# Kernel tuning notes

Measured on AMD Instinct MI355X. Metric: run time of the kernel, lower is better.

The kernel has to match this reference:

```python
import jax, jax.numpy as jnp
import numpy as np

N, F, K, O = 8192, 512, 2, 64
FMIN = jnp.finfo(jnp.float32).min


def setup_inputs() -> dict:
    key = jax.random.key(0)
    k1, k2, k3, k4, k5 = jax.random.split(key, 5)
    H = jax.random.normal(k1, (N, F), dtype=jnp.float32)
    # sparse-ish binary adjacency with self-loops (float mask, as in TF code)
    A = (jax.random.uniform(k2, (N, N)) < 0.0125).astype(jnp.float32)
    A = jnp.maximum(A, jnp.eye(N, dtype=jnp.float32))
    idx = jnp.arange(N, dtype=jnp.int32)
    W = jax.random.normal(k3, (K, F, O), dtype=jnp.float32) * 0.1
    b = jnp.zeros((K, O), dtype=jnp.float32)
    a1 = jax.random.normal(k4, (K, O), dtype=jnp.float32) * 0.1
    a2 = jax.random.normal(k5, (K, O), dtype=jnp.float32) * 0.1
    return {"H": H, "A": A, "idx": idx, "W": W, "b": b, "a1": a1, "a2": a2}


def reference(H, A, idx, W, b, a1, a2):
    # batch_A = tf.gather(A, idx, axis=1)
    batch_A = A[:, idx]                                  # [N, N]
    HW = jnp.einsum('nf,kfo->kno', H, W)                 # [K, N, O]
    attn1 = jnp.einsum('kno,ko->kn', HW, a1)             # [K, N]
    attn2 = jnp.einsum('kno,ko->kn', HW, a2)             # [K, N]
    # transpose(meshgrid sum): scores[k, i, j] = attn1[k, i] + attn2[k, j]
    scores = attn1[:, :, None] + attn2[:, None, :]       # [K, N, N]
    scores = scores + FMIN * (1.0 - batch_A)[None]
    scores = jnp.where(scores >= 0, scores, 0.2 * scores)  # LeakyReLU(0.2)
    attn = jax.nn.softmax(scores, axis=-1)               # [K, N, N]
    # res = transpose(HW^T @ attn) => res[k, i] = sum_j attn[k, j, i] * HW[k, j]
    res = jnp.einsum('kji,kjo->kio', attn, HW)           # [K, N, O]
    out = jax.nn.relu(res + b[:, None, :])               # [K, N, O]
    # concat heads along feature axis
    return jnp.transpose(out, (1, 0, 2)).reshape(N, K * O)
```

## Files before the change

### kernel.cpp

```cpp
#include <hip/hip_runtime.h>

#define NN 8192
#define FD 512
typedef unsigned long long u64;

__device__ __forceinline__ unsigned f2bf(float x) {
  unsigned u = __float_as_uint(x);
  u += 0x7FFFu + ((u >> 16) & 1u);
  return u >> 16;
}

__device__ __forceinline__ u64 xpose64(u64 x, int lane) {
  const u64 M[6] = {0x00000000FFFFFFFFULL, 0x0000FFFF0000FFFFULL,
                    0x00FF00FF00FF00FFULL, 0x0F0F0F0F0F0F0F0FULL,
                    0x3333333333333333ULL, 0x5555555555555555ULL};
  int d = 32;
#pragma unroll
  for (int s = 0; s < 6; ++s, d >>= 1) {
    u64 y = __shfl_xor(x, d);
    const u64 ML = M[s], MH = ~ML;
    if ((lane & d) == 0) x = (x & ML) | ((y & ML) << d);
    else                 x = (x & MH) | ((y & MH) >> d);
  }
  return x;
}

__global__ __launch_bounds__(256) void kA(
    const float* __restrict__ H, const float* __restrict__ W,
    const float* __restrict__ a1, const float* __restrict__ a2,
    const float* __restrict__ A, const int* __restrict__ idx,
    unsigned* __restrict__ hw2, float* __restrict__ c1,
    float* __restrict__ c2p, u64* __restrict__ rmask_t) {
  __shared__ u64 sm[4][128];
  __shared__ int sbad;
  const int wv = threadIdx.x >> 6, lane = threadIdx.x & 63;
  if (blockIdx.x < 512) {
    const int nbase = __builtin_amdgcn_readfirstlane(blockIdx.x * 16 + wv * 4);
    const float* __restrict__ W0 = W;
    const float* __restrict__ W1 = W + FD * 64;
    float acc0[4] = {0.f, 0.f, 0.f, 0.f};
    float acc1[4] = {0.f, 0.f, 0.f, 0.f};
    float4 hc[4], hn[4];
#pragma unroll
    for (int r = 0; r < 4; ++r)
      hc[r] = *(const float4*)(H + (size_t)(nbase + r) * FD);
    for (int f = 0; f < FD; f += 4) {
      if (f + 4 < FD) {
#pragma unroll
        for (int r = 0; r < 4; ++r)
          hn[r] = *(const float4*)(H + (size_t)(nbase + r) * FD + f + 4);
      }
      const float w00 = W0[(f+0)*64 + lane], w01 = W0[(f+1)*64 + lane];
      const float w02 = W0[(f+2)*64 + lane], w03 = W0[(f+3)*64 + lane];
      const float w10 = W1[(f+0)*64 + lane], w11 = W1[(f+1)*64 + lane];
      const float w12 = W1[(f+2)*64 + lane], w13 = W1[(f+3)*64 + lane];
#pragma unroll
      for (int r = 0; r < 4; ++r) {
        acc0[r] = fmaf(hc[r].x, w00, acc0[r]);
        acc0[r] = fmaf(hc[r].y, w01, acc0[r]);
        acc0[r] = fmaf(hc[r].z, w02, acc0[r]);
        acc0[r] = fmaf(hc[r].w, w03, acc0[r]);
        acc1[r] = fmaf(hc[r].x, w10, acc1[r]);
        acc1[r] = fmaf(hc[r].y, w11, acc1[r]);
        acc1[r] = fmaf(hc[r].z, w12, acc1[r]);
        acc1[r] = fmaf(hc[r].w, w13, acc1[r]);
      }
#pragma unroll
      for (int r = 0; r < 4; ++r) hc[r] = hn[r];
    }
    const float a10 = a1[lane],      a20 = a2[lane];
    const float a11 = a1[64 + lane], a21 = a2[64 + lane];
#pragma unroll
    for (int r = 0; r < 4; ++r) {
      const int n = nbase + r;
      hw2[(size_t)n * 64 + lane] = f2bf(acc0[r]) | (f2bf(acc1[r]) << 16);
      float s10 = acc0[r] * a10;
      float s20 = acc0[r] * a20;
      float s11 = acc1[r] * a11;
      float s21 = acc1[r] * a21;
#pragma unroll
      for (int off = 32; off; off >>= 1) {
        s10 += __shfl_down(s10, off);
        s20 += __shfl_down(s20, off);
        s11 += __shfl_down(s11, off);
        s21 += __shfl_down(s21, off);
      }
      if (lane == 0) {
        c1[n]          = s10;
        c1[NN + n]     = s11;
        c2p[n * 2]     = s20;
        c2p[n * 2 + 1] = s21;
      }
    }
    return;
  }
  const int bs = blockIdx.x - 512;
  const int j = bs * 4 + wv;
  if (threadIdx.x == 0) sbad = 0;
  __syncthreads();
  {
    bool bad = false;
    const int4* __restrict__ idx4 = (const int4*)idx;
#pragma unroll
    for (int p = 0; p < 8; ++p) {
      const int t = threadIdx.x + p * 256;
      const int4 v = idx4[t];
      const int b0 = t * 4;
      bad |= (v.x != b0) | (v.y != b0 + 1) | (v.z != b0 + 2) | (v.w != b0 + 3);
    }
    if (__ballot(bad) != 0ULL && lane == 0) sbad = 1;
  }
  __syncthreads();
  const bool fast = (sbad == 0);
  const float* __restrict__ Arow = A + (size_t)j * NN;

  float4 cur[4], nxt[4];
  {
    const int cb = lane * 4;
    if (fast) {
#pragma unroll
      for (int p = 0; p < 4; ++p) cur[p] = *(const float4*)(Arow + cb + p * 256);
    } else {
#pragma unroll
      for (int p = 0; p < 4; ++p) {
        const int c0 = cb + p * 256;
        cur[p].x = Arow[idx[c0 + 0]]; cur[p].y = Arow[idx[c0 + 1]];
        cur[p].z = Arow[idx[c0 + 2]]; cur[p].w = Arow[idx[c0 + 3]];
      }
    }
  }
  for (int g = 0; g < 8; ++g) {
    if (g < 7) {
      const int cb = (g + 1) * 1024 + lane * 4;
      if (fast) {
#pragma unroll
        for (int p = 0; p < 4; ++p) nxt[p] = *(const float4*)(Arow + cb + p * 256);
      } else {
#pragma unroll
        for (int p = 0; p < 4; ++p) {
          const int c0 = cb + p * 256;
          nxt[p].x = Arow[idx[c0 + 0]]; nxt[p].y = Arow[idx[c0 + 1]];
          nxt[p].z = Arow[idx[c0 + 2]]; nxt[p].w = Arow[idx[c0 + 3]];
        }
      }
    }
#pragma unroll
    for (int p = 0; p < 4; ++p) {
      const float av[4] = {cur[p].x, cur[p].y, cur[p].z, cur[p].w};
#pragma unroll
      for (int q = 0; q < 4; ++q) {
        const u64 bal = __ballot(av[q] != 0.f);
        if (lane == 0) sm[wv][g * 16 + p * 4 + q] = bal;
      }
    }
#pragma unroll
    for (int p = 0; p < 4; ++p) cur[p] = nxt[p];
  }
  __syncthreads();
  {
    const int t = threadIdx.x;
    const int w = t >> 1;
    const int jj = (t & 1) * 2;
    ulonglong2 v;
    v.x = sm[jj + 0][w];
    v.y = sm[jj + 1][w];
    *(ulonglong2*)(rmask_t + (size_t)w * NN + bs * 4 + jj) = v;
  }
}

__global__ __launch_bounds__(256) void kB(
    const u64* __restrict__ rmask_t, const float* __restrict__ c1,
    const float* __restrict__ c2p, unsigned short* __restrict__ edges16,
    unsigned char* __restrict__ ecnt8, float2* __restrict__ p2) {
  __shared__ unsigned short seg[4][64][24];
  __shared__ int scnt[4][64];
  const int wv = threadIdx.x >> 6, lane = threadIdx.x & 63;
  if (blockIdx.x < 512) {
    const int w = blockIdx.x >> 2;
    const int q = blockIdx.x & 3;
    const int base = ((w >> 4) << 10) + (((w >> 2) & 3) << 8) + (w & 3);
    const u64* __restrict__ src = rmask_t + (size_t)w * NN + q * 2048 + wv * 512;
    int cnt = 0;
    u64 x = src[lane];
    for (int jt = 0; jt < 8; ++jt) {
      const u64 nx = (jt < 7) ? src[(jt + 1) * 64 + lane] : 0ULL;
      x = xpose64(x, lane);
      const int jb = q * 2048 + wv * 512 + jt * 64;
      while (x) {
        const int r = __builtin_ctzll(x);
        x &= x - 1;
        if (cnt < 24) seg[wv][lane][cnt] = (unsigned short)(jb + r);
        ++cnt;
      }
      x = nx;
    }
    scnt[wv][lane] = min(cnt, 24);
    __syncthreads();
    for (int rr = 0; rr < 16; ++rr) {
      const int r = wv * 16 + rr;
      const int i = base + 4 * r;
      const int s0c = scnt[0][r], s1c = scnt[1][r];
      const int s2c = scnt[2][r], s3c = scnt[3][r];
      const int o1 = s0c, o2 = o1 + s1c, o3 = o2 + s2c;
      const int tot = min(o3 + s3c, 64);
      const int pos = lane;
      if (pos < tot) {
        int s, off;
        if (pos < o1)      { s = 0; off = pos; }
        else if (pos < o2) { s = 1; off = pos - o1; }
        else if (pos < o3) { s = 2; off = pos - o2; }
        else               { s = 3; off = pos - o3; }
        edges16[(size_t)i * 256 + q * 64 + pos] = seg[s][r][off];
      }
      if (lane == 0) ecnt8[i * 4 + q] = (unsigned char)tot;
    }
    return;
  }
  const int j = (blockIdx.x - 512) * 4 + wv;
  const float c10 = c1[j];
  const float c11 = c1[NN + j];
  float s0 = 0.f, s1 = 0.f;
#pragma unroll
  for (int h = 0; h < 2; ++h) {
    const int w = lane + h * 64;
    u64 m = rmask_t[(size_t)w * NN + j];
    const int cbase = ((w >> 4) << 10) + (((w >> 2) & 3) << 8) + (w & 3);
    while (m) {
      const int r = __builtin_ctzll(m);
      m &= m - 1;
      const float2 cv = *(const float2*)(c2p + (cbase + 4 * r) * 2);
      float v0 = c10 + cv.x; v0 = (v0 >= 0.f) ? v0 : 0.2f * v0;
      s0 += __expf(v0);
      float v1 = c11 + cv.y; v1 = (v1 >= 0.f) ? v1 : 0.2f * v1;
      s1 += __expf(v1);
    }
  }
#pragma unroll
  for (int off = 32; off; off >>= 1) {
    s0 += __shfl_down(s0, off);
    s1 += __shfl_down(s1, off);
  }
  if (lane == 0) {
    const float I0 = (s0 > 0.f) ? 1.f / s0 : 0.f;
    const float I1 = (s1 > 0.f) ? 1.f / s1 : 0.f;
    *(float4*)(p2 + (size_t)j * 2) = make_float4(c10, I0, c11, I1);
  }
}

__global__ __launch_bounds__(256) void kC(
    const unsigned char* __restrict__ ecnt8, const unsigned short* __restrict__ edges16,
    const float2* __restrict__ p2, const float* __restrict__ c2p,
    const unsigned* __restrict__ hw2, const float* __restrict__ b,
    float* __restrict__ out) {
  const int lane = threadIdx.x & 63;
  const int i = __builtin_amdgcn_readfirstlane(blockIdx.x * 4 + (threadIdx.x >> 6));
  const float c20 = c2p[i * 2];
  const float c21 = c2p[i * 2 + 1];
  const uchar4 c4 = *(const uchar4*)(ecnt8 + (size_t)i * 4);
  const int cq[4] = {c4.x, c4.y, c4.z, c4.w};
  float acc0 = 0.f, acc1 = 0.f;
#pragma unroll
  for (int q = 0; q < 4; ++q) {
    const int cnt = cq[q];
    const unsigned short* __restrict__ e = edges16 + (size_t)i * 256 + q * 64;
    int t = 0;
    for (; t + 4 <= cnt; t += 4) {
      const ushort4 jv = *(const ushort4*)(e + t);
      const int ja = jv.x, jb = jv.y, jc = jv.z, jd = jv.w;
      const float4 pa = *(const float4*)(p2 + (size_t)ja * 2);
      const float4 pb = *(const float4*)(p2 + (size_t)jb * 2);
      const float4 pc = *(const float4*)(p2 + (size_t)jc * 2);
      const float4 pd = *(const float4*)(p2 + (size_t)jd * 2);
      const unsigned ua = hw2[ja * 64 + lane];
      const unsigned ub = hw2[jb * 64 + lane];
      const unsigned uc = hw2[jc * 64 + lane];
      const unsigned ud = hw2[jd * 64 + lane];
      float v, w;
      v = pa.x + c20; v = (v >= 0.f) ? v : 0.2f * v; w = __expf(v) * pa.y;
      acc0 = fmaf(w, __uint_as_float(ua << 16), acc0);
      v = pa.z + c21; v = (v >= 0.f) ? v : 0.2f * v; w = __expf(v) * pa.w;
      acc1 = fmaf(w, __uint_as_float(ua & 0xFFFF0000u), acc1);
      v = pb.x + c20; v = (v >= 0.f) ? v : 0.2f * v; w = __expf(v) * pb.y;
      acc0 = fmaf(w, __uint_as_float(ub << 16), acc0);
      v = pb.z + c21; v = (v >= 0.f) ? v : 0.2f * v; w = __expf(v) * pb.w;
      acc1 = fmaf(w, __uint_as_float(ub & 0xFFFF0000u), acc1);
      v = pc.x + c20; v = (v >= 0.f) ? v : 0.2f * v; w = __expf(v) * pc.y;
      acc0 = fmaf(w, __uint_as_float(uc << 16), acc0);
      v = pc.z + c21; v = (v >= 0.f) ? v : 0.2f * v; w = __expf(v) * pc.w;
      acc1 = fmaf(w, __uint_as_float(uc & 0xFFFF0000u), acc1);
      v = pd.x + c20; v = (v >= 0.f) ? v : 0.2f * v; w = __expf(v) * pd.y;
      acc0 = fmaf(w, __uint_as_float(ud << 16), acc0);
      v = pd.z + c21; v = (v >= 0.f) ? v : 0.2f * v; w = __expf(v) * pd.w;
      acc1 = fmaf(w, __uint_as_float(ud & 0xFFFF0000u), acc1);
    }
    for (; t < cnt; ++t) {
      const int j = e[t];
      const float4 p = *(const float4*)(p2 + (size_t)j * 2);
      const unsigned u = hw2[j * 64 + lane];
      float v0 = p.x + c20; v0 = (v0 >= 0.f) ? v0 : 0.2f * v0;
      float w0 = __expf(v0) * p.y;
      float v1 = p.z + c21; v1 = (v1 >= 0.f) ? v1 : 0.2f * v1;
      float w1 = __expf(v1) * p.w;
      acc0 = fmaf(w0, __uint_as_float(u << 16), acc0);
      acc1 = fmaf(w1, __uint_as_float(u & 0xFFFF0000u), acc1);
    }
  }
  out[(size_t)i * 128 + lane]      = fmaxf(acc0 + b[lane], 0.f);
  out[(size_t)i * 128 + 64 + lane] = fmaxf(acc1 + b[64 + lane], 0.f);
}

extern "C" void kernel_launch(void* const* d_in, const int* in_sizes, int n_in,
                              void* d_out, int out_size, void* d_ws, size_t ws_size,
                              hipStream_t stream) {
  const float* H   = (const float*)d_in[0];
  const float* A   = (const float*)d_in[1];
  const int*   idx = (const int*)d_in[2];
  const float* W   = (const float*)d_in[3];
  const float* b   = (const float*)d_in[4];
  const float* a1  = (const float*)d_in[5];
  const float* a2  = (const float*)d_in[6];
  float* out = (float*)d_out;

  char* ws = (char*)d_ws;
  unsigned*       hw2     = (unsigned*)(ws + 0);
  float*          c1      = (float*)(ws + 2097152);
  float*          c2p     = (float*)(ws + 2162688);
  float2*         p2      = (float2*)(ws + 2228224);
  u64*            rmask_t = (u64*)(ws + 2359296);
  unsigned short* edges16 = (unsigned short*)(ws + 10747904);
  unsigned char*  ecnt8   = (unsigned char*)(ws + 14942208);
  (void)in_sizes; (void)n_in; (void)out_size; (void)ws_size;

  kA<<<2560, 256, 0, stream>>>(H, W, a1, a2, A, idx, hw2, c1, c2p, rmask_t);
  kB<<<2560, 256, 0, stream>>>(rmask_t, c1, c2p, edges16, ecnt8, p2);
  kC<<<2048, 256, 0, stream>>>(ecnt8, edges16, p2, c2p, hw2, b, out);
}
```

Measured before the change: 448.5 us.

## Restructure into four kernels, fuse row-sum into mask build, nontemporal A loads

Splits the projection and the mask building into separate kernels, with a single block computing the identity-index check once and storing it as a flag. The softmax denominator is now computed in the mask-building kernel from the shared-memory ballot masks, so it no longer rereads rmask_t from global memory. A is streamed with nontemporal loads to avoid polluting the cache. In exchange there is one extra launch and a serialized dependency: the projection must finish before the mask pass can start.

```diff
diff --git a/kernel.cpp b/kernel.cpp
--- a/kernel.cpp
+++ b/kernel.cpp
@@ -3,6 +3,13 @@
 #define NN 8192
 #define FD 512
 typedef unsigned long long u64;
+
+typedef float __attribute__((ext_vector_type(4))) f4v;
+
+__device__ __forceinline__ float4 ntld4(const float* p) {
+  f4v v = __builtin_nontemporal_load((const f4v*)p);
+  return make_float4(v.x, v.y, v.z, v.w);
+}
 
 __device__ __forceinline__ unsigned f2bf(float x) {
   unsigned u = __float_as_uint(x);
@@ -25,80 +32,15 @@
   return x;
 }
 
-__global__ __launch_bounds__(256) void kA(
+__global__ __launch_bounds__(256) void k1(
     const float* __restrict__ H, const float* __restrict__ W,
     const float* __restrict__ a1, const float* __restrict__ a2,
-    const float* __restrict__ A, const int* __restrict__ idx,
+    const int* __restrict__ idx,
     unsigned* __restrict__ hw2, float* __restrict__ c1,
-    float* __restrict__ c2p, u64* __restrict__ rmask_t) {
-  __shared__ u64 sm[4][128];
-  __shared__ int sbad;
+    float* __restrict__ c2p, int* __restrict__ flag) {
   const int wv = threadIdx.x >> 6, lane = threadIdx.x & 63;
-  if (blockIdx.x < 512) {
-    const int nbase = __builtin_amdgcn_readfirstlane(blockIdx.x * 16 + wv * 4);
-    const float* __restrict__ W0 = W;
-    const float* __restrict__ W1 = W + FD * 64;
-    float acc0[4] = {0.f, 0.f, 0.f, 0.f};
-    float acc1[4] = {0.f, 0.f, 0.f, 0.f};
-    float4 hc[4], hn[4];
-#pragma unroll
-    for (int r = 0; r < 4; ++r)
-      hc[r] = *(const float4*)(H + (size_t)(nbase + r) * FD);
-    for (int f = 0; f < FD; f += 4) {
-      if (f + 4 < FD) {
-#pragma unroll
-        for (int r = 0; r < 4; ++r)
-          hn[r] = *(const float4*)(H + (size_t)(nbase + r) * FD + f + 4);
-      }
-      const float w00 = W0[(f+0)*64 + lane], w01 = W0[(f+1)*64 + lane];
-      const float w02 = W0[(f+2)*64 + lane], w03 = W0[(f+3)*64 + lane];
-      const float w10 = W1[(f+0)*64 + lane], w11 = W1[(f+1)*64 + lane];
-      const float w12 = W1[(f+2)*64 + lane], w13 = W1[(f+3)*64 + lane];
-#pragma unroll
-      for (int r = 0; r < 4; ++r) {
-        acc0[r] = fmaf(hc[r].x, w00, acc0[r]);
-        acc0[r] = fmaf(hc[r].y, w01, acc0[r]);
-        acc0[r] = fmaf(hc[r].z, w02, acc0[r]);
-        acc0[r] = fmaf(hc[r].w, w03, acc0[r]);
-        acc1[r] = fmaf(hc[r].x, w10, acc1[r]);
-        acc1[r] = fmaf(hc[r].y, w11, acc1[r]);
-        acc1[r] = fmaf(hc[r].z, w12, acc1[r]);
-        acc1[r] = fmaf(hc[r].w, w13, acc1[r]);
-      }
-#pragma unroll
-      for (int r = 0; r < 4; ++r) hc[r] = hn[r];
-    }
-    const float a10 = a1[lane],      a20 = a2[lane];
-    const float a11 = a1[64 + lane], a21 = a2[64 + lane];
-#pragma unroll
-    for (int r = 0; r < 4; ++r) {
-      const int n = nbase + r;
-      hw2[(size_t)n * 64 + lane] = f2bf(acc0[r]) | (f2bf(acc1[r]) << 16);
-      float s10 = acc0[r] * a10;
-      float s20 = acc0[r] * a20;
-      float s11 = acc1[r] * a11;
-      float s21 = acc1[r] * a21;
-#pragma unroll
-      for (int off = 32; off; off >>= 1) {
-        s10 += __shfl_down(s10, off);
-        s20 += __shfl_down(s20, off);
-        s11 += __shfl_down(s11, off);
-        s21 += __shfl_down(s21, off);
-      }
-      if (lane == 0) {
-        c1[n]          = s10;
-        c1[NN + n]     = s11;
-        c2p[n * 2]     = s20;
-        c2p[n * 2 + 1] = s21;
-      }
-    }
-    return;
-  }
-  const int bs = blockIdx.x - 512;
-  const int j = bs * 4 + wv;
-  if (threadIdx.x == 0) sbad = 0;
-  __syncthreads();
-  {
+  if (blockIdx.x == 512) {
+    __shared__ int bad4[4];
     bool bad = false;
     const int4* __restrict__ idx4 = (const int4*)idx;
 #pragma unroll
@@ -108,10 +50,80 @@
       const int b0 = t * 4;
       bad |= (v.x != b0) | (v.y != b0 + 1) | (v.z != b0 + 2) | (v.w != b0 + 3);
     }
-    if (__ballot(bad) != 0ULL && lane == 0) sbad = 1;
-  }
-  __syncthreads();
-  const bool fast = (sbad == 0);
+    if (lane == 0) bad4[wv] = (__ballot(bad) != 0ULL) ? 1 : 0;
+    __syncthreads();
+    if (threadIdx.x == 0) flag[0] = bad4[0] | bad4[1] | bad4[2] | bad4[3];
+    return;
+  }
+  const int nbase = __builtin_amdgcn_readfirstlane(blockIdx.x * 16 + wv * 4);
+  const float* __restrict__ W0 = W;
+  const float* __restrict__ W1 = W + FD * 64;
+  float acc0[4] = {0.f, 0.f, 0.f, 0.f};
+  float acc1[4] = {0.f, 0.f, 0.f, 0.f};
+  float4 hc[4], hn[4];
+#pragma unroll
+  for (int r = 0; r < 4; ++r)
+    hc[r] = *(const float4*)(H + (size_t)(nbase + r) * FD);
+  for (int f = 0; f < FD; f += 4) {
+    if (f + 4 < FD) {
+#pragma unroll
+      for (int r = 0; r < 4; ++r)
+        hn[r] = *(const float4*)(H + (size_t)(nbase + r) * FD + f + 4);
+    }
+    const float w00 = W0[(f+0)*64 + lane], w01 = W0[(f+1)*64 + lane];
+    const float w02 = W0[(f+2)*64 + lane], w03 = W0[(f+3)*64 + lane];
+    const float w10 = W1[(f+0)*64 + lane], w11 = W1[(f+1)*64 + lane];
+    const float w12 = W1[(f+2)*64 + lane], w13 = W1[(f+3)*64 + lane];
+#pragma unroll
+    for (int r = 0; r < 4; ++r) {
+      acc0[r] = fmaf(hc[r].x, w00, acc0[r]);
+      acc0[r] = fmaf(hc[r].y, w01, acc0[r]);
+      acc0[r] = fmaf(hc[r].z, w02, acc0[r]);
+      acc0[r] = fmaf(hc[r].w, w03, acc0[r]);
+      acc1[r] = fmaf(hc[r].x, w10, acc1[r]);
+      acc1[r] = fmaf(hc[r].y, w11, acc1[r]);
+      acc1[r] = fmaf(hc[r].z, w12, acc1[r]);
+      acc1[r] = fmaf(hc[r].w, w13, acc1[r]);
+    }
+#pragma unroll
+    for (int r = 0; r < 4; ++r) hc[r] = hn[r];
+  }
+  const float a10 = a1[lane],      a20 = a2[lane];
+  const float a11 = a1[64 + lane], a21 = a2[64 + lane];
+#pragma unroll
+  for (int r = 0; r < 4; ++r) {
+    const int n = nbase + r;
+    hw2[(size_t)n * 64 + lane] = f2bf(acc0[r]) | (f2bf(acc1[r]) << 16);
+    float s10 = acc0[r] * a10;
+    float s20 = acc0[r] * a20;
+    float s11 = acc1[r] * a11;
+    float s21 = acc1[r] * a21;
+#pragma unroll
+    for (int off = 32; off; off >>= 1) {
+      s10 += __shfl_down(s10, off);
+      s20 += __shfl_down(s20, off);
+      s11 += __shfl_down(s11, off);
+      s21 += __shfl_down(s21, off);
+    }
+    if (lane == 0) {
+      c1[n]          = s10;
+      c1[NN + n]     = s11;
+      c2p[n * 2]     = s20;
+      c2p[n * 2 + 1] = s21;
+    }
+  }
+}
+
+__global__ __launch_bounds__(256) void k2(
+    const float* __restrict__ A, const int* __restrict__ idx,
+    const int* __restrict__ flag, const float* __restrict__ c1,
+    const float* __restrict__ c2p,
+    u64* __restrict__ rmask_t, float2* __restrict__ p2) {
+  __shared__ u64 sm[4][128];
+  const int wv = threadIdx.x >> 6, lane = threadIdx.x & 63;
+  const int bs = blockIdx.x;
+  const int j = bs * 4 + wv;
+  const bool fast = (flag[0] == 0);
   const float* __restrict__ Arow = A + (size_t)j * NN;
 
   float4 cur[4], nxt[4];
@@ -119,7 +131,7 @@
     const int cb = lane * 4;
     if (fast) {
 #pragma unroll
-      for (int p = 0; p < 4; ++p) cur[p] = *(const float4*)(Arow + cb + p * 256);
+      for (int p = 0; p < 4; ++p) cur[p] = ntld4(Arow + cb + p * 256);
     } else {
 #pragma unroll
       for (int p = 0; p < 4; ++p) {
@@ -134,7 +146,7 @@
       const int cb = (g + 1) * 1024 + lane * 4;
       if (fast) {
 #pragma unroll
-        for (int p = 0; p < 4; ++p) nxt[p] = *(const float4*)(Arow + cb + p * 256);
+        for (int p = 0; p < 4; ++p) nxt[p] = ntld4(Arow + cb + p * 256);
       } else {
 #pragma unroll
         for (int p = 0; p < 4; ++p) {
@@ -166,64 +178,13 @@
     v.y = sm[jj + 1][w];
     *(ulonglong2*)(rmask_t + (size_t)w * NN + bs * 4 + jj) = v;
   }
-}
-
-__global__ __launch_bounds__(256) void kB(
-    const u64* __restrict__ rmask_t, const float* __restrict__ c1,
-    const float* __restrict__ c2p, unsigned short* __restrict__ edges16,
-    unsigned char* __restrict__ ecnt8, float2* __restrict__ p2) {
-  __shared__ unsigned short seg[4][64][24];
-  __shared__ int scnt[4][64];
-  const int wv = threadIdx.x >> 6, lane = threadIdx.x & 63;
-  if (blockIdx.x < 512) {
-    const int w = blockIdx.x >> 2;
-    const int q = blockIdx.x & 3;
-    const int base = ((w >> 4) << 10) + (((w >> 2) & 3) << 8) + (w & 3);
-    const u64* __restrict__ src = rmask_t + (size_t)w * NN + q * 2048 + wv * 512;
-    int cnt = 0;
-    u64 x = src[lane];
-    for (int jt = 0; jt < 8; ++jt) {
-      const u64 nx = (jt < 7) ? src[(jt + 1) * 64 + lane] : 0ULL;
-      x = xpose64(x, lane);
-      const int jb = q * 2048 + wv * 512 + jt * 64;
-      while (x) {
-        const int r = __builtin_ctzll(x);
-        x &= x - 1;
-        if (cnt < 24) seg[wv][lane][cnt] = (unsigned short)(jb + r);
-        ++cnt;
-      }
-      x = nx;
-    }
-    scnt[wv][lane] = min(cnt, 24);
-    __syncthreads();
-    for (int rr = 0; rr < 16; ++rr) {
-      const int r = wv * 16 + rr;
-      const int i = base + 4 * r;
-      const int s0c = scnt[0][r], s1c = scnt[1][r];
-      const int s2c = scnt[2][r], s3c = scnt[3][r];
-      const int o1 = s0c, o2 = o1 + s1c, o3 = o2 + s2c;
-      const int tot = min(o3 + s3c, 64);
-      const int pos = lane;
-      if (pos < tot) {
-        int s, off;
-        if (pos < o1)      { s = 0; off = pos; }
-        else if (pos < o2) { s = 1; off = pos - o1; }
-        else if (pos < o3) { s = 2; off = pos - o2; }
-        else               { s = 3; off = pos - o3; }
-        edges16[(size_t)i * 256 + q * 64 + pos] = seg[s][r][off];
-      }
-      if (lane == 0) ecnt8[i * 4 + q] = (unsigned char)tot;
-    }
-    return;
-  }
-  const int j = (blockIdx.x - 512) * 4 + wv;
   const float c10 = c1[j];
   const float c11 = c1[NN + j];
   float s0 = 0.f, s1 = 0.f;
 #pragma unroll
   for (int h = 0; h < 2; ++h) {
     const int w = lane + h * 64;
-    u64 m = rmask_t[(size_t)w * NN + j];
+    u64 m = sm[wv][w];
     const int cbase = ((w >> 4) << 10) + (((w >> 2) & 3) << 8) + (w & 3);
     while (m) {
       const int r = __builtin_ctzll(m);
@@ -247,7 +208,53 @@
   }
 }
 
-__global__ __launch_bounds__(256) void kC(
+__global__ __launch_bounds__(256) void k3(
+    const u64* __restrict__ rmask_t, unsigned short* __restrict__ edges16,
+    unsigned char* __restrict__ ecnt8) {
+  __shared__ unsigned short seg[4][64][24];
+  __shared__ int scnt[4][64];
+  const int wv = threadIdx.x >> 6, lane = threadIdx.x & 63;
+  const int w = blockIdx.x >> 2;
+  const int q = blockIdx.x & 3;
+  const int base = ((w >> 4) << 10) + (((w >> 2) & 3) << 8) + (w & 3);
+  const u64* __restrict__ src = rmask_t + (size_t)w * NN + q * 2048 + wv * 512;
+  int cnt = 0;
+  u64 x = src[lane];
+  for (int jt = 0; jt < 8; ++jt) {
+    const u64 nx = (jt < 7) ? src[(jt + 1) * 64 + lane] : 0ULL;
+    x = xpose64(x, lane);
+    const int jb = q * 2048 + wv * 512 + jt * 64;
+    while (x) {
+      const int r = __builtin_ctzll(x);
+      x &= x - 1;
+      if (cnt < 24) seg[wv][lane][cnt] = (unsigned short)(jb + r);
+      ++cnt;
+    }
+    x = nx;
+  }
+  scnt[wv][lane] = min(cnt, 24);
+  __syncthreads();
+  for (int rr = 0; rr < 16; ++rr) {
+    const int r = wv * 16 + rr;
+    const int i = base + 4 * r;
+    const int s0c = scnt[0][r], s1c = scnt[1][r];
+    const int s2c = scnt[2][r], s3c = scnt[3][r];
+    const int o1 = s0c, o2 = o1 + s1c, o3 = o2 + s2c;
+    const int tot = min(o3 + s3c, 64);
+    const int pos = lane;
+    if (pos < tot) {
+      int s, off;
+      if (pos < o1)      { s = 0; off = pos; }
+      else if (pos < o2) { s = 1; off = pos - o1; }
+      else if (pos < o3) { s = 2; off = pos - o2; }
+      else               { s = 3; off = pos - o3; }
+      edges16[(size_t)i * 256 + q * 64 + pos] = seg[s][r][off];
+    }
+    if (lane == 0) ecnt8[i * 4 + q] = (unsigned char)tot;
+  }
+}
+
+__global__ __launch_bounds__(256) void k4(
     const unsigned char* __restrict__ ecnt8, const unsigned short* __restrict__ edges16,
     const float2* __restrict__ p2, const float* __restrict__ c2p,
     const unsigned* __restrict__ hw2, const float* __restrict__ b,
@@ -326,12 +333,14 @@
   float*          c1      = (float*)(ws + 2097152);
   float*          c2p     = (float*)(ws + 2162688);
   float2*         p2      = (float2*)(ws + 2228224);
-  u64*            rmask_t = (u64*)(ws + 2359296);
-  unsigned short* edges16 = (unsigned short*)(ws + 10747904);
-  unsigned char*  ecnt8   = (unsigned char*)(ws + 14942208);
+  int*            flag    = (int*)(ws + 2359296);
+  u64*            rmask_t = (u64*)(ws + 2359552);
+  unsigned short* edges16 = (unsigned short*)(ws + 10748160);
+  unsigned char*  ecnt8   = (unsigned char*)(ws + 14942464);
   (void)in_sizes; (void)n_in; (void)out_size; (void)ws_size;
 
-  kA<<<2560, 256, 0, stream>>>(H, W, a1, a2, A, idx, hw2, c1, c2p, rmask_t);
-  kB<<<2560, 256, 0, stream>>>(rmask_t, c1, c2p, edges16, ecnt8, p2);
-  kC<<<2048, 256, 0, stream>>>(ecnt8, edges16, p2, c2p, hw2, b, out);
-}
+  k1<<<513, 256, 0, stream>>>(H, W, a1, a2, idx, hw2, c1, c2p, flag);
+  k2<<<2048, 256, 0, stream>>>(A, idx, flag, c1, c2p, rmask_t, p2);
+  k3<<<512, 256, 0, stream>>>(rmask_t, edges16, ecnt8);
+  k4<<<2048, 256, 0, stream>>>(ecnt8, edges16, p2, c2p, hw2, b, out);
+}
```

After: 457.0 us. Within noise of the previous version (+1.9%).
